# Performance work log

Hardware: AMD Instinct MI355X
Metric: run time of the kernel (lower is better)

## Reference

```python
import jax, jax.numpy as jnp
import numpy as np

B, S, H, T = 64, 512, 768, 400


def setup_inputs() -> dict:
    key = jax.random.key(0)
    k1, k2 = jax.random.split(key)
    hidden = jax.random.normal(k1, (B, S, H), dtype=jnp.float32)
    # word_ids: non-decreasing piece->word map per sample, like HF tokenizer word_ids()
    word_ids = jnp.sort(jax.random.randint(k2, (B, S), 0, T), axis=-1).astype(jnp.int32)
    return {"hidden": hidden, "word_ids": word_ids, "num_tokens": T}


def reference(hidden, word_ids, num_tokens):
    # Ragged segment mean-pool: pool subword pieces into per-word reps.
    # hidden: [B, S, H] float; word_ids: [B, S] int in [0, num_tokens)
    b, s, h = hidden.shape
    # Flatten (sample, word) into one global segment id: sample*T + word
    seg = (jnp.arange(b, dtype=word_ids.dtype)[:, None] * num_tokens + word_ids).reshape(-1)
    sums = jax.ops.segment_sum(hidden.reshape(b * s, h), seg, num_segments=b * num_tokens)
    counts = jax.ops.segment_sum(jnp.ones((b * s,), hidden.dtype), seg, num_segments=b * num_tokens)
    # Words with zero pieces -> sum 0 / 1 = 0, matching torch.zeros fallback
    pooled = sums / jnp.maximum(counts, 1.0)[:, None]
    return pooled.reshape(b, num_tokens, h)
```

## Files before the change

### kernel.cpp

```cpp
#include <hip/hip_runtime.h>


#define BB 64
#define SS 512
#define HH 768
#define TT 400

__global__ __launch_bounds__(64) void bert_lattice_pool_kernel(
    const float* __restrict__ hidden,
    const int* __restrict__ word_ids,
    float* __restrict__ out)
{
    const int bt = blockIdx.x;
    const int b  = bt / TT;
    const int t  = bt - b * TT;

    const int* wrow = word_ids + b * SS;

    int lo = 0, hi = SS;
    while (lo < hi) {
        int mid = (lo + hi) >> 1;
        if (wrow[mid] < t) lo = mid + 1; else hi = mid;
    }
    const int start = lo;
    hi = SS;
    while (lo < hi) {
        int mid = (lo + hi) >> 1;
        if (wrow[mid] <= t) lo = mid + 1; else hi = mid;
    }
    const int end   = lo;
    const int count = end - start;

    const int lane = threadIdx.x;

    float4 acc0 = make_float4(0.f, 0.f, 0.f, 0.f);
    float4 acc1 = make_float4(0.f, 0.f, 0.f, 0.f);
    float4 acc2 = make_float4(0.f, 0.f, 0.f, 0.f);

    for (int s = start; s < end; ++s) {
        const float4* p =
            reinterpret_cast<const float4*>(hidden + ((size_t)b * SS + s) * HH);
        float4 v0 = p[lane];
        float4 v1 = p[lane + 64];
        float4 v2 = p[lane + 128];
        acc0.x += v0.x; acc0.y += v0.y; acc0.z += v0.z; acc0.w += v0.w;
        acc1.x += v1.x; acc1.y += v1.y; acc1.z += v1.z; acc1.w += v1.w;
        acc2.x += v2.x; acc2.y += v2.y; acc2.z += v2.z; acc2.w += v2.w;
    }

    const float inv = 1.0f / (float)(count > 0 ? count : 1);

    float4* o = reinterpret_cast<float4*>(out + ((size_t)b * TT + t) * HH);
    float4 r0 = make_float4(acc0.x * inv, acc0.y * inv, acc0.z * inv, acc0.w * inv);
    float4 r1 = make_float4(acc1.x * inv, acc1.y * inv, acc1.z * inv, acc1.w * inv);
    float4 r2 = make_float4(acc2.x * inv, acc2.y * inv, acc2.z * inv, acc2.w * inv);
    o[lane]       = r0;
    o[lane + 64]  = r1;
    o[lane + 128] = r2;
}

extern "C" void kernel_launch(void* const* d_in, const int* in_sizes, int n_in,
                              void* d_out, int out_size, void* d_ws, size_t ws_size,
                              hipStream_t stream) {
    (void)in_sizes; (void)n_in; (void)d_ws; (void)ws_size; (void)out_size;
    const float* hidden   = (const float*)d_in[0];
    const int*   word_ids = (const int*)d_in[1];
    float*       out      = (float*)d_out;

    dim3 grid(BB * TT);
    dim3 block(64);
    bert_lattice_pool_kernel<<<grid, block, 0, stream>>>(hidden, word_ids, out);
}
```

Baseline: 176.0 us.

## Pool four words per block with shared word_ids and shared segment bounds

Each 256-thread block now handles four consecutive words, one wavefront per word, instead of one word per 64-thread block. The block stages the sample's word_ids row in LDS, and five threads each run one lower-bound search to produce shared segment boundaries, replacing two global-memory binary searches per word. This cuts block count and redundant index lookups. It adds two barriers, and the four wavefronts may carry unequal work. TT divisible by RPB keeps each block inside one sample.

```diff
diff --git a/kernel.cpp b/kernel.cpp
--- a/kernel.cpp
+++ b/kernel.cpp
@@ -5,33 +5,40 @@
 #define SS 512
 #define HH 768
 #define TT 400
+#define RPB 4
 
-__global__ __launch_bounds__(64) void bert_lattice_pool_kernel(
+__global__ __launch_bounds__(256) void bert_lattice_pool_kernel(
     const float* __restrict__ hidden,
     const int* __restrict__ word_ids,
     float* __restrict__ out)
 {
-    const int bt = blockIdx.x;
-    const int b  = bt / TT;
-    const int t  = bt - b * TT;
+    const int row0 = blockIdx.x * RPB;
+    const int b    = row0 / TT;
+    const int t0   = row0 - b * TT;
 
-    const int* wrow = word_ids + b * SS;
+    __shared__ int s_w[SS];
+    __shared__ int s_bounds[RPB + 1];
 
-    int lo = 0, hi = SS;
-    while (lo < hi) {
-        int mid = (lo + hi) >> 1;
-        if (wrow[mid] < t) lo = mid + 1; else hi = mid;
+    const int2* wrow2 = reinterpret_cast<const int2*>(word_ids + b * SS);
+    reinterpret_cast<int2*>(s_w)[threadIdx.x] = wrow2[threadIdx.x];
+    __syncthreads();
+
+    if (threadIdx.x <= RPB) {
+        const int t = t0 + threadIdx.x;
+        int lo = 0, hi = SS;
+        while (lo < hi) {
+            int mid = (lo + hi) >> 1;
+            if (s_w[mid] < t) lo = mid + 1; else hi = mid;
+        }
+        s_bounds[threadIdx.x] = lo;
     }
-    const int start = lo;
-    hi = SS;
-    while (lo < hi) {
-        int mid = (lo + hi) >> 1;
-        if (wrow[mid] <= t) lo = mid + 1; else hi = mid;
-    }
-    const int end   = lo;
+    __syncthreads();
+
+    const int wv    = threadIdx.x >> 6;
+    const int lane  = threadIdx.x & 63;
+    const int start = s_bounds[wv];
+    const int end   = s_bounds[wv + 1];
     const int count = end - start;
-
-    const int lane = threadIdx.x;
 
     float4 acc0 = make_float4(0.f, 0.f, 0.f, 0.f);
     float4 acc1 = make_float4(0.f, 0.f, 0.f, 0.f);
@@ -50,7 +57,7 @@
 
     const float inv = 1.0f / (float)(count > 0 ? count : 1);
 
-    float4* o = reinterpret_cast<float4*>(out + ((size_t)b * TT + t) * HH);
+    float4* o = reinterpret_cast<float4*>(out + ((size_t)(row0 + wv)) * HH);
     float4 r0 = make_float4(acc0.x * inv, acc0.y * inv, acc0.z * inv, acc0.w * inv);
     float4 r1 = make_float4(acc1.x * inv, acc1.y * inv, acc1.z * inv, acc1.w * inv);
     float4 r2 = make_float4(acc2.x * inv, acc2.y * inv, acc2.z * inv, acc2.w * inv);
@@ -67,7 +74,7 @@
     const int*   word_ids = (const int*)d_in[1];
     float*       out      = (float*)d_out;
 
-    dim3 grid(BB * TT);
-    dim3 block(64);
+    dim3 grid((BB * TT) / RPB);
+    dim3 block(256);
     bert_lattice_pool_kernel<<<grid, block, 0, stream>>>(hidden, word_ids, out);
 }
```

Measured after the change: 174.9 us. Within noise of the previous version (-0.6%).
